# Kernel tuning notes

Hardware: AMD Instinct MI355X
Metric: run time of the kernel (lower is better)

The kernel has to match this reference:

```python
import jax, jax.numpy as jnp
import numpy as np

BN_EPS = 1e-5


def _bn(h, gamma, beta, mean, var):
    return (h - mean) * jax.lax.rsqrt(var + BN_EPS) * gamma + beta


def _gin_conv(x, edge_index, edge_weight, Wa, ba, g, be, m, v, Wb, bb):
    # GINConv: (1+eps)*x + sum_j w_ij * x_j, eps=0; then MLP: Linear->BN->ReLU->Linear
    src, dst = edge_index[0], edge_index[1]
    msg = x[src] * edge_weight[:, None]                      # [E, C]
    agg = jax.ops.segment_sum(msg, dst, num_segments=x.shape[0])  # [N, C]
    h = x + agg
    h = h @ Wa + ba
    h = jax.nn.relu(_bn(h, g, be, m, v))
    return h @ Wb + bb


def setup_inputs() -> dict:
    key = jax.random.key(0)
    ks = jax.random.split(key, 16)
    N, E, C_IN, C_OUT, H = 100000, 1600000, 128, 64, 32
    x = jax.random.normal(ks[0], (N, C_IN), dtype=jnp.float32)
    edge_index = jax.random.randint(ks[1], (2, E), 0, N, dtype=jnp.int32)
    edge_weight = jax.random.uniform(ks[2], (E,), dtype=jnp.float32)
    s1 = 1.0 / np.sqrt(C_IN)
    s2 = 1.0 / np.sqrt(H)
    return {
        "x": x,
        "edge_weight": edge_weight,
        "W1a": jax.random.normal(ks[3], (C_IN, H), dtype=jnp.float32) * s1,
        "b1a": jnp.zeros((H,), jnp.float32),
        "g1": jnp.ones((H,), jnp.float32),
        "be1": jnp.zeros((H,), jnp.float32),
        "m1": jax.random.normal(ks[4], (H,), dtype=jnp.float32) * 0.1,
        "v1": jax.random.uniform(ks[5], (H,), dtype=jnp.float32) + 0.5,
        "W1b": jax.random.normal(ks[6], (H, H), dtype=jnp.float32) * s2,
        "b1b": jnp.zeros((H,), jnp.float32),
        "W2a": jax.random.normal(ks[7], (H, C_OUT), dtype=jnp.float32) * s2,
        "b2a": jnp.zeros((C_OUT,), jnp.float32),
        "g2": jnp.ones((C_OUT,), jnp.float32),
        "be2": jnp.zeros((C_OUT,), jnp.float32),
        "m2": jax.random.normal(ks[8], (C_OUT,), dtype=jnp.float32) * 0.1,
        "v2": jax.random.uniform(ks[9], (C_OUT,), dtype=jnp.float32) + 0.5,
        "W2b": jax.random.normal(ks[10], (C_OUT, C_OUT), dtype=jnp.float32) * (1.0 / np.sqrt(C_OUT)),
        "b2b": jnp.zeros((C_OUT,), jnp.float32),
        "edge_index": edge_index,
    }


def reference(x, edge_weight, W1a, b1a, g1, be1, m1, v1, W1b, b1b,
              W2a, b2a, g2, be2, m2, v2, W2b, b2b, edge_index):
    # eval mode: dropout(p=0.6) is identity, BN uses running stats
    h = jax.nn.relu(_gin_conv(x, edge_index, edge_weight,
                              W1a, b1a, g1, be1, m1, v1, W1b, b1b))
    out = _gin_conv(h, edge_index, edge_weight,
                    W2a, b2a, g2, be2, m2, v2, W2b, b2b)
    return out
```

## Files before the change

kernel.cpp:

```cpp
#include <hip/hip_runtime.h>


#define BN_EPS 1e-5f
#define BKT 128
#define BKT_SH 7
#define EPB 4096
#define MAXB 800
#define LDS_E 2560

typedef __attribute__((ext_vector_type(8))) short bf16x8;
typedef __attribute__((ext_vector_type(4))) float f32x4v;

__device__ __forceinline__ unsigned short f2bf(float f) {
    unsigned u = __float_as_uint(f);
    return (unsigned short)((u + 0x7FFFu + ((u >> 16) & 1u)) >> 16);
}
__device__ __forceinline__ float bflo(unsigned u) { return __uint_as_float(u << 16); }
__device__ __forceinline__ float bfhi(unsigned u) { return __uint_as_float(u & 0xFFFF0000u); }

__device__ __forceinline__ void gacc8(uint4 v, float w, float* acc) {
    acc[0] += bflo(v.x) * w; acc[1] += bfhi(v.x) * w;
    acc[2] += bflo(v.y) * w; acc[3] += bfhi(v.y) * w;
    acc[4] += bflo(v.z) * w; acc[5] += bfhi(v.z) * w;
    acc[6] += bflo(v.w) * w; acc[7] += bfhi(v.w) * w;
}

__device__ __forceinline__ void gather_seg8(const unsigned short* __restrict__ tab,
                                            const int2* __restrict__ epack,
                                            int e, int end, int c0, float* acc) {
    long long q0 = 0, q1 = 0, q2 = 0, q3 = 0;
    if (e + 4 <= end) {
        q0 = __builtin_nontemporal_load((const long long*)&epack[e + 0]);
        q1 = __builtin_nontemporal_load((const long long*)&epack[e + 1]);
        q2 = __builtin_nontemporal_load((const long long*)&epack[e + 2]);
        q3 = __builtin_nontemporal_load((const long long*)&epack[e + 3]);
    }
    for (; e + 8 <= end; e += 4) {
        int s0 = (int)q0, s1 = (int)q1, s2 = (int)q2, s3 = (int)q3;
        float w0 = __int_as_float((int)(q0 >> 32));
        float w1 = __int_as_float((int)(q1 >> 32));
        float w2 = __int_as_float((int)(q2 >> 32));
        float w3 = __int_as_float((int)(q3 >> 32));
        uint4 v0 = *(const uint4*)&tab[(size_t)s0 * 32 + c0];
        uint4 v1 = *(const uint4*)&tab[(size_t)s1 * 32 + c0];
        uint4 v2 = *(const uint4*)&tab[(size_t)s2 * 32 + c0];
        uint4 v3 = *(const uint4*)&tab[(size_t)s3 * 32 + c0];
        q0 = __builtin_nontemporal_load((const long long*)&epack[e + 4]);
        q1 = __builtin_nontemporal_load((const long long*)&epack[e + 5]);
        q2 = __builtin_nontemporal_load((const long long*)&epack[e + 6]);
        q3 = __builtin_nontemporal_load((const long long*)&epack[e + 7]);
        gacc8(v0, w0, acc); gacc8(v1, w1, acc);
        gacc8(v2, w2, acc); gacc8(v3, w3, acc);
    }
    if (e + 4 <= end) {
        int s0 = (int)q0, s1 = (int)q1, s2 = (int)q2, s3 = (int)q3;
        float w0 = __int_as_float((int)(q0 >> 32));
        float w1 = __int_as_float((int)(q1 >> 32));
        float w2 = __int_as_float((int)(q2 >> 32));
        float w3 = __int_as_float((int)(q3 >> 32));
        uint4 v0 = *(const uint4*)&tab[(size_t)s0 * 32 + c0];
        uint4 v1 = *(const uint4*)&tab[(size_t)s1 * 32 + c0];
        uint4 v2 = *(const uint4*)&tab[(size_t)s2 * 32 + c0];
        uint4 v3 = *(const uint4*)&tab[(size_t)s3 * 32 + c0];
        gacc8(v0, w0, acc); gacc8(v1, w1, acc);
        gacc8(v2, w2, acc); gacc8(v3, w3, acc);
        e += 4;
    }
    for (; e < end; ++e) {
        long long q = __builtin_nontemporal_load((const long long*)&epack[e]);
        int sn = (int)q;
        float w = __int_as_float((int)(q >> 32));
        uint4 v = *(const uint4*)&tab[(size_t)sn * 32 + c0];
        gacc8(v, w, acc);
    }
}

__global__ __launch_bounds__(256) void gemm1_kernel(const float* __restrict__ x,
                                                    const float* __restrict__ W,
                                                    unsigned short* __restrict__ y1b,
                                                    int* __restrict__ gcur,
                                                    int N, int ncur) {
    __shared__ unsigned short wbT[32][136];
    int t = threadIdx.x;
    if (t == 0) {
        int b0 = blockIdx.x * 16;
        #pragma unroll
        for (int j = 0; j < 16; ++j)
            if (b0 + j < ncur) gcur[b0 + j] = 0;
    }
    for (int i = t; i < 4096; i += 256) {
        int k = i >> 5, c = i & 31;
        wbT[c][k] = f2bf(W[i]);
    }
    __syncthreads();
    int wid = t >> 6, lane = t & 63;
    int lr = lane & 15, lg = lane >> 4;
    int arow = blockIdx.x * 64 + wid * 16 + lr;
    int xr = min(arow, N - 1);
    bf16x8 bf[4][2];
    #pragma unroll
    for (int s = 0; s < 4; ++s) {
        int kb = s * 32 + lg * 8;
        bf[s][0] = *(const bf16x8*)&wbT[lr][kb];
        bf[s][1] = *(const bf16x8*)&wbT[16 + lr][kb];
    }
    f32x4v acc0 = {0.f, 0.f, 0.f, 0.f};
    f32x4v acc1 = {0.f, 0.f, 0.f, 0.f};
    #pragma unroll
    for (int s = 0; s < 4; ++s) {
        const float* xp = &x[(size_t)xr * 128 + s * 32 + lg * 8];
        float4 xa = *(const float4*)xp;
        float4 xb = *(const float4*)(xp + 4);
        bf16x8 af;
        af[0] = (short)f2bf(xa.x); af[1] = (short)f2bf(xa.y);
        af[2] = (short)f2bf(xa.z); af[3] = (short)f2bf(xa.w);
        af[4] = (short)f2bf(xb.x); af[5] = (short)f2bf(xb.y);
        af[6] = (short)f2bf(xb.z); af[7] = (short)f2bf(xb.w);
        acc0 = __builtin_amdgcn_mfma_f32_16x16x32_bf16(af, bf[s][0], acc0, 0, 0, 0);
        acc1 = __builtin_amdgcn_mfma_f32_16x16x32_bf16(af, bf[s][1], acc1, 0, 0, 0);
    }
    int rowbase = blockIdx.x * 64 + wid * 16 + lg * 4;
    #pragma unroll
    for (int r = 0; r < 4; ++r) {
        int orow = rowbase + r;
        if (orow < N) {
            y1b[(size_t)orow * 32 + lr]      = f2bf(acc0[r]);
            y1b[(size_t)orow * 32 + 16 + lr] = f2bf(acc1[r]);
        }
    }
}

__global__ __launch_bounds__(512) void stage_kernel(const int* __restrict__ ei,
                                                    const float* __restrict__ ew,
                                                    int* __restrict__ gcur,
                                                    int2* __restrict__ staged,
                                                    int E, int cap, int NBUCK) {
    __shared__ int hist[MAXB], base_[MAXB], curs[MAXB];
    __shared__ int gbase[MAXB];
    __shared__ int2 data[EPB];
    __shared__ unsigned short bslot[EPB];
    int t  = threadIdx.x;
    int e0 = blockIdx.x * EPB;
    int cnt = min(EPB, E - e0);
    for (int i = t; i < MAXB; i += 512) hist[i] = 0;
    __syncthreads();
    for (int i = t; i < cnt; i += 512) {
        int d = ei[(size_t)E + e0 + i];
        atomicAdd(&hist[d >> BKT_SH], 1);
    }
    __syncthreads();
    int lo = t * 2;
    int v0 = (lo + 0 < MAXB) ? hist[lo + 0] : 0;
    int v1 = (lo + 1 < MAXB) ? hist[lo + 1] : 0;
    int s = v0 + v1;
    gbase[t] = s;
    __syncthreads();
    for (int off = 1; off < 512; off <<= 1) {
        int y = (t >= off) ? gbase[t - off] : 0;
        __syncthreads();
        gbase[t] += y;
        __syncthreads();
    }
    int excl = gbase[t] - s;
    if (lo + 0 < MAXB) { base_[lo + 0] = excl; curs[lo + 0] = excl; }
    excl += v0;
    if (lo + 1 < MAXB) { base_[lo + 1] = excl; curs[lo + 1] = excl; }
    __syncthreads();
    for (int i = t; i < cnt; i += 512) {
        int sn = ei[e0 + i];
        int d  = ei[(size_t)E + e0 + i];
        float w = ew[e0 + i];
        int b = d >> BKT_SH, dl = d & (BKT - 1);
        int pos = atomicAdd(&curs[b], 1);
        data[pos]  = make_int2((dl << 20) | sn, __float_as_int(w));
        bslot[pos] = (unsigned short)b;
    }
    __syncthreads();
    for (int b = t; b < NBUCK; b += 512) {
        int c = hist[b];
        gbase[b] = c ? atomicAdd(&gcur[b * 16], c) : 0;
    }
    __syncthreads();
    for (int i = t; i < cnt; i += 512) {
        int b  = bslot[i];
        int gp = gbase[b] + (i - base_[b]);
        if (gp < cap) staged[(size_t)b * cap + gp] = data[i];
    }
}

__global__ __launch_bounds__(256) void refill_kernel(const int2* __restrict__ staged,
                                                     const int* __restrict__ gcur,
                                                     int2* __restrict__ epack,
                                                     int2* __restrict__ row_se,
                                                     int N, int cap) {
    __shared__ int2 ebuf[LDS_E];
    __shared__ int hist[BKT];
    __shared__ int curs[BKT];
    int b = blockIdx.x, t = threadIdx.x;
    int cnt  = min(gcur[b * 16], cap);
    int base = b * cap;
    size_t e0 = (size_t)b * cap;
    if (t < BKT) hist[t] = 0;
    __syncthreads();
    for (int i = t; i < cnt; i += 256) {
        int2 p = staged[e0 + i];
        ebuf[i] = p;
        atomicAdd(&hist[p.x >> 20], 1);
    }
    __syncthreads();
    if (t < BKT) curs[t] = hist[t];
    __syncthreads();
    for (int off = 1; off < BKT; off <<= 1) {
        int y = (t < BKT && t >= off) ? curs[t - off] : 0;
        __syncthreads();
        if (t < BKT) curs[t] += y;
        __syncthreads();
    }
    if (t < BKT) {
        int excl = curs[t] - hist[t];
        int node = (b << BKT_SH) + t;
        if (node < N) row_se[node] = make_int2(base + excl, base + excl + hist[t]);
        curs[t] = excl;
    }
    __syncthreads();
    for (int i = t; i < cnt; i += 256) {
        int2 p = ebuf[i];
        int dl = p.x >> 20;
        int pos = base + atomicAdd(&curs[dl], 1);
        epack[pos] = make_int2(p.x & 0xFFFFF, p.y);
    }
}

__global__ __launch_bounds__(256) void layer1_kernel(
    const unsigned short* __restrict__ y1b, const int2* __restrict__ row_se,
    const int2* __restrict__ epack,
    const float* __restrict__ b1a, const float* __restrict__ g1,
    const float* __restrict__ be1, const float* __restrict__ m1,
    const float* __restrict__ v1, const float* __restrict__ W1b,
    const float* __restrict__ b1b, unsigned short* __restrict__ h1b, int N) {
    __shared__ float w1b[1024];
    __shared__ float t1s[64][33];
    int t = threadIdx.x;
    for (int i = t; i < 1024; i += 256) w1b[i] = W1b[i];
    __syncthreads();
    int g = t >> 2, l = t & 3;
    int node = blockIdx.x * 64 + g;
    int c0 = l << 3;
    bool act = node < N;
    float acc[8] = {0.f, 0.f, 0.f, 0.f, 0.f, 0.f, 0.f, 0.f};
    if (act) {
        int2 se = row_se[node];
        uint4 sv = *(const uint4*)&y1b[(size_t)node * 32 + c0];
        gather_seg8(y1b, epack, se.x, se.y, c0, acc);
        gacc8(sv, 1.f, acc);
        #pragma unroll
        for (int j = 0; j < 8; ++j) {
            int c = c0 + j;
            float scale = g1[c] * rsqrtf(v1[c] + BN_EPS);
            t1s[g][c] = fmaxf((acc[j] + b1a[c] - m1[c]) * scale + be1[c], 0.f);
        }
    }
    asm volatile("" ::: "memory");
    if (act) {
        float a[8];
        #pragma unroll
        for (int j = 0; j < 8; ++j) a[j] = b1b[c0 + j];
        #pragma unroll
        for (int k = 0; k < 32; ++k) {
            float tv = t1s[g][k];
            const float* wr = &w1b[k * 32 + c0];
            #pragma unroll
            for (int j = 0; j < 8; ++j) a[j] += tv * wr[j];
        }
        unsigned long long p0 = 0, p1 = 0;
        #pragma unroll
        for (int j = 0; j < 4; ++j)
            p0 |= (unsigned long long)f2bf(fmaxf(a[j], 0.f)) << (16 * j);
        #pragma unroll
        for (int j = 0; j < 4; ++j)
            p1 |= (unsigned long long)f2bf(fmaxf(a[4 + j], 0.f)) << (16 * j);
        __builtin_nontemporal_store(p0, (unsigned long long*)&h1b[(size_t)node * 32 + c0 + 0]);
        __builtin_nontemporal_store(p1, (unsigned long long*)&h1b[(size_t)node * 32 + c0 + 4]);
    }
}

__global__ __launch_bounds__(256) void layer2a_kernel(
    const unsigned short* __restrict__ h1b, const int2* __restrict__ row_se,
    const int2* __restrict__ epack,
    const float* __restrict__ W2a, const float* __restrict__ b2a,
    const float* __restrict__ g2, const float* __restrict__ be2,
    const float* __restrict__ m2, const float* __restrict__ v2,
    unsigned short* __restrict__ t2b, int N) {
    __shared__ float w2a[2048];
    __shared__ float s1s[64][33];
    __shared__ float sc2s[64], sh2s[64];
    int t = threadIdx.x;
    for (int i = t; i < 2048; i += 256) w2a[i] = W2a[i];
    if (t < 64) {
        float sc = g2[t] * rsqrtf(v2[t] + BN_EPS);
        sc2s[t] = sc;
        sh2s[t] = (b2a[t] - m2[t]) * sc + be2[t];
    }
    __syncthreads();
    int g = t >> 2, l = t & 3;
    int node = blockIdx.x * 64 + g;
    int c0 = l << 3;
    bool act = node < N;
    float acc[8] = {0.f, 0.f, 0.f, 0.f, 0.f, 0.f, 0.f, 0.f};
    if (act) {
        int2 se = row_se[node];
        uint4 sv = *(const uint4*)&h1b[(size_t)node * 32 + c0];
        gather_seg8(h1b, epack, se.x, se.y, c0, acc);
        gacc8(sv, 1.f, acc);
        #pragma unroll
        for (int j = 0; j < 8; ++j) s1s[g][c0 + j] = acc[j];
    }
    asm volatile("" ::: "memory");
    if (act) {
        int d0 = l << 4;
        float a[16];
        #pragma unroll
        for (int j = 0; j < 16; ++j) a[j] = 0.f;
        #pragma unroll
        for (int k = 0; k < 32; ++k) {
            float sv = s1s[g][k];
            const float* wr = &w2a[k * 64 + d0];
            #pragma unroll
            for (int j = 0; j < 16; ++j) a[j] += sv * wr[j];
        }
        unsigned long long pk[4] = {0, 0, 0, 0};
        #pragma unroll
        for (int j = 0; j < 16; ++j) {
            int c = d0 + j;
            float o = fmaxf(a[j] * sc2s[c] + sh2s[c], 0.f);
            pk[j >> 2] |= (unsigned long long)f2bf(o) << (16 * (j & 3));
        }
        #pragma unroll
        for (int q = 0; q < 4; ++q)
            __builtin_nontemporal_store(pk[q],
                (unsigned long long*)&t2b[(size_t)node * 64 + d0 + 4 * q]);
    }
}

__global__ __launch_bounds__(256) void final_kernel(const unsigned short* __restrict__ t2b,
                                                    const float* __restrict__ W2b,
                                                    const float* __restrict__ b2b,
                                                    float* __restrict__ out, int N) {
    __shared__ float w2b[4096];
    __shared__ float t2s[32][68];
    int t = threadIdx.x;
    for (int i = t; i < 4096; i += 256) w2b[i] = W2b[i];
    int g = t >> 3, l = t & 7;
    int node = blockIdx.x * 32 + g;
    int c0 = l << 3;
    bool act = node < N;
    if (act) {
        uint4 v = *(const uint4*)&t2b[(size_t)node * 64 + c0];
        t2s[g][c0 + 0] = bflo(v.x); t2s[g][c0 + 1] = bfhi(v.x);
        t2s[g][c0 + 2] = bflo(v.y); t2s[g][c0 + 3] = bfhi(v.y);
        t2s[g][c0 + 4] = bflo(v.z); t2s[g][c0 + 5] = bfhi(v.z);
        t2s[g][c0 + 6] = bflo(v.w); t2s[g][c0 + 7] = bfhi(v.w);
    }
    __syncthreads();
    if (act) {
        float a[8];
        #pragma unroll
        for (int j = 0; j < 8; ++j) a[j] = b2b[c0 + j];
        #pragma unroll 8
        for (int k = 0; k < 64; ++k) {
            float tv = t2s[g][k];
            const float* wr = &w2b[k * 64 + c0];
            float4 w0 = *(const float4*)wr;
            float4 w1 = *(const float4*)(wr + 4);
            a[0] += tv * w0.x; a[1] += tv * w0.y; a[2] += tv * w0.z; a[3] += tv * w0.w;
            a[4] += tv * w1.x; a[5] += tv * w1.y; a[6] += tv * w1.z; a[7] += tv * w1.w;
        }
        *(float4*)&out[(size_t)node * 64 + c0 + 0] = *(float4*)&a[0];
        *(float4*)&out[(size_t)node * 64 + c0 + 4] = *(float4*)&a[4];
    }
}

extern "C" void kernel_launch(void* const* d_in, const int* in_sizes, int n_in,
                              void* d_out, int out_size, void* d_ws, size_t ws_size,
                              hipStream_t stream) {
    const float* x   = (const float*)d_in[0];
    const float* ew  = (const float*)d_in[1];
    const float* W1a = (const float*)d_in[2];
    const float* b1a = (const float*)d_in[3];
    const float* g1  = (const float*)d_in[4];
    const float* be1 = (const float*)d_in[5];
    const float* m1  = (const float*)d_in[6];
    const float* v1  = (const float*)d_in[7];
    const float* W1b = (const float*)d_in[8];
    const float* b1b = (const float*)d_in[9];
    const float* W2a = (const float*)d_in[10];
    const float* b2a = (const float*)d_in[11];
    const float* g2  = (const float*)d_in[12];
    const float* be2 = (const float*)d_in[13];
    const float* m2  = (const float*)d_in[14];
    const float* v2  = (const float*)d_in[15];
    const float* W2b = (const float*)d_in[16];
    const float* b2b = (const float*)d_in[17];
    const int*   ei  = (const int*)d_in[18];

    const int N = in_sizes[0] / 128;
    const int E = in_sizes[1];
    const int NBUCK = (N + BKT - 1) >> BKT_SH;
    const int NCUR  = NBUCK * 16;

    unsigned short* y1b = (unsigned short*)d_ws;
    int2*  row_se  = (int2*)(y1b + (size_t)N * 32);
    int*   gcur    = (int*)(row_se + N);
    int2*  epack   = (int2*)(gcur + NCUR + 16);
    size_t fixed_bytes = (char*)epack - (char*)d_ws;
    size_t avail = (ws_size > fixed_bytes) ? (ws_size - fixed_bytes) : 0;
    int cap = (int)((avail / (2 * sizeof(int2))) / NBUCK);
    cap &= ~63;
    if (cap > LDS_E) cap = LDS_E;
    int2* staged = epack + (size_t)NBUCK * cap;
    unsigned short* h1b = (unsigned short*)staged;
    unsigned short* t2b = h1b + (size_t)N * 32;

    gemm1_kernel<<<(N + 63) / 64, 256, 0, stream>>>(x, W1a, y1b, gcur, N, NCUR);
    stage_kernel<<<(E + EPB - 1) / EPB, 512, 0, stream>>>(ei, ew, gcur, staged, E, cap, NBUCK);
    refill_kernel<<<NBUCK, 256, 0, stream>>>(staged, gcur, epack, row_se, N, cap);
    layer1_kernel<<<(N + 63) / 64, 256, 0, stream>>>(y1b, row_se, epack,
                                                     b1a, g1, be1, m1, v1, W1b, b1b, h1b, N);
    layer2a_kernel<<<(N + 63) / 64, 256, 0, stream>>>(h1b, row_se, epack,
                                                      W2a, b2a, g2, be2, m2, v2, t2b, N);
    final_kernel<<<(N + 31) / 32, 256, 0, stream>>>(t2b, W2b, b2b, (float*)d_out, N);
}
```

Baseline: 150.1 us.

## Merge first GEMM and edge staging into one block-specialized kernel

The bf16 MFMA x@W1a projection and the edge bucketing/staging pass are combined into one launch. Blocks below G_STAGE do staging and the rest do the GEMM, with shared memory overlaid through a union. The two independent stages can then run concurrently on the GPU, and one kernel launch and its tail are removed. Zeroing the gcur counters moves from the GEMM kernel to a hipMemsetAsync, which adds a small memset operation. The union sizes every block to the staging kernel's large LDS footprint, so GEMM blocks now run at 512 threads with lower occupancy.

```diff
diff --git a/kernel.cpp b/kernel.cpp
--- a/kernel.cpp
+++ b/kernel.cpp
@@ -75,116 +75,115 @@
     }
 }
 
-__global__ __launch_bounds__(256) void gemm1_kernel(const float* __restrict__ x,
-                                                    const float* __restrict__ W,
-                                                    unsigned short* __restrict__ y1b,
-                                                    int* __restrict__ gcur,
-                                                    int N, int ncur) {
-    __shared__ unsigned short wbT[32][136];
+union SMem {
+    struct {
+        int hist[MAXB], base_[MAXB], curs[MAXB], gbase[MAXB];
+        int2 data[EPB];
+        unsigned short bslot[EPB];
+    } st;
+    struct { unsigned short wbT[32][136]; } gm;
+};
+
+__global__ __launch_bounds__(512) void gs_kernel(const float* __restrict__ x,
+                                                 const float* __restrict__ W,
+                                                 unsigned short* __restrict__ y1b,
+                                                 const int* __restrict__ ei,
+                                                 const float* __restrict__ ew,
+                                                 int* __restrict__ gcur,
+                                                 int2* __restrict__ staged,
+                                                 int N, int E, int cap, int NBUCK,
+                                                 int G_STAGE) {
+    __shared__ SMem sm;
     int t = threadIdx.x;
-    if (t == 0) {
-        int b0 = blockIdx.x * 16;
-        #pragma unroll
-        for (int j = 0; j < 16; ++j)
-            if (b0 + j < ncur) gcur[b0 + j] = 0;
-    }
-    for (int i = t; i < 4096; i += 256) {
-        int k = i >> 5, c = i & 31;
-        wbT[c][k] = f2bf(W[i]);
-    }
-    __syncthreads();
-    int wid = t >> 6, lane = t & 63;
-    int lr = lane & 15, lg = lane >> 4;
-    int arow = blockIdx.x * 64 + wid * 16 + lr;
-    int xr = min(arow, N - 1);
-    bf16x8 bf[4][2];
-    #pragma unroll
-    for (int s = 0; s < 4; ++s) {
-        int kb = s * 32 + lg * 8;
-        bf[s][0] = *(const bf16x8*)&wbT[lr][kb];
-        bf[s][1] = *(const bf16x8*)&wbT[16 + lr][kb];
-    }
-    f32x4v acc0 = {0.f, 0.f, 0.f, 0.f};
-    f32x4v acc1 = {0.f, 0.f, 0.f, 0.f};
-    #pragma unroll
-    for (int s = 0; s < 4; ++s) {
-        const float* xp = &x[(size_t)xr * 128 + s * 32 + lg * 8];
-        float4 xa = *(const float4*)xp;
-        float4 xb = *(const float4*)(xp + 4);
-        bf16x8 af;
-        af[0] = (short)f2bf(xa.x); af[1] = (short)f2bf(xa.y);
-        af[2] = (short)f2bf(xa.z); af[3] = (short)f2bf(xa.w);
-        af[4] = (short)f2bf(xb.x); af[5] = (short)f2bf(xb.y);
-        af[6] = (short)f2bf(xb.z); af[7] = (short)f2bf(xb.w);
-        acc0 = __builtin_amdgcn_mfma_f32_16x16x32_bf16(af, bf[s][0], acc0, 0, 0, 0);
-        acc1 = __builtin_amdgcn_mfma_f32_16x16x32_bf16(af, bf[s][1], acc1, 0, 0, 0);
-    }
-    int rowbase = blockIdx.x * 64 + wid * 16 + lg * 4;
-    #pragma unroll
-    for (int r = 0; r < 4; ++r) {
-        int orow = rowbase + r;
-        if (orow < N) {
-            y1b[(size_t)orow * 32 + lr]      = f2bf(acc0[r]);
-            y1b[(size_t)orow * 32 + 16 + lr] = f2bf(acc1[r]);
-        }
-    }
-}
-
-__global__ __launch_bounds__(512) void stage_kernel(const int* __restrict__ ei,
-                                                    const float* __restrict__ ew,
-                                                    int* __restrict__ gcur,
-                                                    int2* __restrict__ staged,
-                                                    int E, int cap, int NBUCK) {
-    __shared__ int hist[MAXB], base_[MAXB], curs[MAXB];
-    __shared__ int gbase[MAXB];
-    __shared__ int2 data[EPB];
-    __shared__ unsigned short bslot[EPB];
-    int t  = threadIdx.x;
-    int e0 = blockIdx.x * EPB;
-    int cnt = min(EPB, E - e0);
-    for (int i = t; i < MAXB; i += 512) hist[i] = 0;
-    __syncthreads();
-    for (int i = t; i < cnt; i += 512) {
-        int d = ei[(size_t)E + e0 + i];
-        atomicAdd(&hist[d >> BKT_SH], 1);
-    }
-    __syncthreads();
-    int lo = t * 2;
-    int v0 = (lo + 0 < MAXB) ? hist[lo + 0] : 0;
-    int v1 = (lo + 1 < MAXB) ? hist[lo + 1] : 0;
-    int s = v0 + v1;
-    gbase[t] = s;
-    __syncthreads();
-    for (int off = 1; off < 512; off <<= 1) {
-        int y = (t >= off) ? gbase[t - off] : 0;
-        __syncthreads();
-        gbase[t] += y;
-        __syncthreads();
-    }
-    int excl = gbase[t] - s;
-    if (lo + 0 < MAXB) { base_[lo + 0] = excl; curs[lo + 0] = excl; }
-    excl += v0;
-    if (lo + 1 < MAXB) { base_[lo + 1] = excl; curs[lo + 1] = excl; }
-    __syncthreads();
-    for (int i = t; i < cnt; i += 512) {
-        int sn = ei[e0 + i];
-        int d  = ei[(size_t)E + e0 + i];
-        float w = ew[e0 + i];
-        int b = d >> BKT_SH, dl = d & (BKT - 1);
-        int pos = atomicAdd(&curs[b], 1);
-        data[pos]  = make_int2((dl << 20) | sn, __float_as_int(w));
-        bslot[pos] = (unsigned short)b;
-    }
-    __syncthreads();
-    for (int b = t; b < NBUCK; b += 512) {
-        int c = hist[b];
-        gbase[b] = c ? atomicAdd(&gcur[b * 16], c) : 0;
-    }
-    __syncthreads();
-    for (int i = t; i < cnt; i += 512) {
-        int b  = bslot[i];
-        int gp = gbase[b] + (i - base_[b]);
-        if (gp < cap) staged[(size_t)b * cap + gp] = data[i];
+    if ((int)blockIdx.x < G_STAGE) {
+        int e0 = blockIdx.x * EPB;
+        int cnt = min(EPB, E - e0);
+        for (int i = t; i < MAXB; i += 512) sm.st.hist[i] = 0;
+        __syncthreads();
+        for (int i = t; i < cnt; i += 512) {
+            int d = ei[(size_t)E + e0 + i];
+            atomicAdd(&sm.st.hist[d >> BKT_SH], 1);
+        }
+        __syncthreads();
+        int lo = t * 2;
+        int v0 = (lo + 0 < MAXB) ? sm.st.hist[lo + 0] : 0;
+        int v1 = (lo + 1 < MAXB) ? sm.st.hist[lo + 1] : 0;
+        int s = v0 + v1;
+        sm.st.gbase[t] = s;
+        __syncthreads();
+        for (int off = 1; off < 512; off <<= 1) {
+            int y = (t >= off) ? sm.st.gbase[t - off] : 0;
+            __syncthreads();
+            sm.st.gbase[t] += y;
+            __syncthreads();
+        }
+        int excl = sm.st.gbase[t] - s;
+        if (lo + 0 < MAXB) { sm.st.base_[lo + 0] = excl; sm.st.curs[lo + 0] = excl; }
+        excl += v0;
+        if (lo + 1 < MAXB) { sm.st.base_[lo + 1] = excl; sm.st.curs[lo + 1] = excl; }
+        __syncthreads();
+        for (int i = t; i < cnt; i += 512) {
+            int sn = ei[e0 + i];
+            int d  = ei[(size_t)E + e0 + i];
+            float w = ew[e0 + i];
+            int b = d >> BKT_SH, dl = d & (BKT - 1);
+            int pos = atomicAdd(&sm.st.curs[b], 1);
+            sm.st.data[pos]  = make_int2((dl << 20) | sn, __float_as_int(w));
+            sm.st.bslot[pos] = (unsigned short)b;
+        }
+        __syncthreads();
+        for (int b = t; b < NBUCK; b += 512) {
+            int c = sm.st.hist[b];
+            sm.st.gbase[b] = c ? atomicAdd(&gcur[b * 16], c) : 0;
+        }
+        __syncthreads();
+        for (int i = t; i < cnt; i += 512) {
+            int b  = sm.st.bslot[i];
+            int gp = sm.st.gbase[b] + (i - sm.st.base_[b]);
+            if (gp < cap) staged[(size_t)b * cap + gp] = sm.st.data[i];
+        }
+    } else {
+        int gb = (int)blockIdx.x - G_STAGE;
+        for (int i = t; i < 4096; i += 512) {
+            int k = i >> 5, c = i & 31;
+            sm.gm.wbT[c][k] = f2bf(W[i]);
+        }
+        __syncthreads();
+        int wid = t >> 6, lane = t & 63;
+        int lr = lane & 15, lg = lane >> 4;
+        int arow = gb * 128 + wid * 16 + lr;
+        int xr = min(arow, N - 1);
+        bf16x8 bfr[4][2];
+        #pragma unroll
+        for (int s = 0; s < 4; ++s) {
+            int kb = s * 32 + lg * 8;
+            bfr[s][0] = *(const bf16x8*)&sm.gm.wbT[lr][kb];
+            bfr[s][1] = *(const bf16x8*)&sm.gm.wbT[16 + lr][kb];
+        }
+        f32x4v acc0 = {0.f, 0.f, 0.f, 0.f};
+        f32x4v acc1 = {0.f, 0.f, 0.f, 0.f};
+        #pragma unroll
+        for (int s = 0; s < 4; ++s) {
+            const float* xp = &x[(size_t)xr * 128 + s * 32 + lg * 8];
+            float4 xa = *(const float4*)xp;
+            float4 xb = *(const float4*)(xp + 4);
+            bf16x8 af;
+            af[0] = (short)f2bf(xa.x); af[1] = (short)f2bf(xa.y);
+            af[2] = (short)f2bf(xa.z); af[3] = (short)f2bf(xa.w);
+            af[4] = (short)f2bf(xb.x); af[5] = (short)f2bf(xb.y);
+            af[6] = (short)f2bf(xb.z); af[7] = (short)f2bf(xb.w);
+            acc0 = __builtin_amdgcn_mfma_f32_16x16x32_bf16(af, bfr[s][0], acc0, 0, 0, 0);
+            acc1 = __builtin_amdgcn_mfma_f32_16x16x32_bf16(af, bfr[s][1], acc1, 0, 0, 0);
+        }
+        int rowbase = gb * 128 + wid * 16 + lg * 4;
+        #pragma unroll
+        for (int r = 0; r < 4; ++r) {
+            int orow = rowbase + r;
+            if (orow < N) {
+                y1b[(size_t)orow * 32 + lr]      = f2bf(acc0[r]);
+                y1b[(size_t)orow * 32 + 16 + lr] = f2bf(acc1[r]);
+            }
+        }
     }
 }
 
@@ -407,6 +406,8 @@
     const int E = in_sizes[1];
     const int NBUCK = (N + BKT - 1) >> BKT_SH;
     const int NCUR  = NBUCK * 16;
+    const int G_STAGE = (E + EPB - 1) / EPB;
+    const int G_GEMM  = (N + 127) / 128;
 
     unsigned short* y1b = (unsigned short*)d_ws;
     int2*  row_se  = (int2*)(y1b + (size_t)N * 32);
@@ -421,8 +422,9 @@
     unsigned short* h1b = (unsigned short*)staged;
     unsigned short* t2b = h1b + (size_t)N * 32;
 
-    gemm1_kernel<<<(N + 63) / 64, 256, 0, stream>>>(x, W1a, y1b, gcur, N, NCUR);
-    stage_kernel<<<(E + EPB - 1) / EPB, 512, 0, stream>>>(ei, ew, gcur, staged, E, cap, NBUCK);
+    hipMemsetAsync(gcur, 0, (size_t)NCUR * sizeof(int), stream);
+    gs_kernel<<<G_STAGE + G_GEMM, 512, 0, stream>>>(x, W1a, y1b, ei, ew, gcur, staged,
+                                                    N, E, cap, NBUCK, G_STAGE);
     refill_kernel<<<NBUCK, 256, 0, stream>>>(staged, gcur, epack, row_se, N, cap);
     layer1_kernel<<<(N + 63) / 64, 256, 0, stream>>>(y1b, row_se, epack,
                                                      b1a, g1, be1, m1, v1, W1b, b1b, h1b, N);
```

Measured after the change: 149.4 us, median of 2. Within noise of the previous version (-0.5%).
